# Optimization experiments

Hardware: AMD Instinct MI355X
Metric: run time of the kernel (lower is better)

## Reference

```python
import jax, jax.numpy as jnp
import numpy as np

N_NODES = 100000
N_EDGES = 1600000
N_GRAPHS = 64
IN_DIM = 256
OUT_DIM = 512
H1 = OUT_DIM // 4   # 128
H2 = OUT_DIM // 2   # 256


def glorot(key, shape):
    lim = float(np.sqrt(6.0 / (shape[0] + shape[1])))
    return jax.random.uniform(key, shape, jnp.float32, -lim, lim)


def setup_inputs() -> dict:
    key = jax.random.key(0)
    ks = jax.random.split(key, 8)
    x = jax.random.normal(ks[0], (N_NODES, IN_DIM), jnp.float32)
    edge_index = jax.random.randint(ks[1], (2, N_EDGES), 0, N_NODES, jnp.int64)
    batch = jnp.sort(jax.random.randint(ks[2], (N_NODES,), 0, N_GRAPHS, jnp.int64))
    return {
        'x': x,
        'edge_index': edge_index,
        'batch': batch,
        'W1': glorot(ks[3], (IN_DIM, H1)),
        'b1': jnp.zeros((H1,), jnp.float32),
        'W2': glorot(ks[4], (H1, H2)),
        'b2': jnp.zeros((H2,), jnp.float32),
        'fc_W': glorot(ks[5], (H2, OUT_DIM)),
        'fc_b': jnp.zeros((OUT_DIM,), jnp.float32),
    }


def gcn_conv(x, W, b, src, dst, n_nodes):
    # PyG GCNConv (default): add self-loops, sym-normalized aggregation of XW + bias
    h = x @ W                                   # [N, F_out] transform first (cheaper gather)
    ones = jnp.ones((src.shape[0],), h.dtype)
    deg = jax.ops.segment_sum(ones, dst, num_segments=n_nodes)  # includes self-loops
    dinv = jax.lax.rsqrt(jnp.maximum(deg, 1.0))
    norm = dinv[src] * dinv[dst]                # [E]
    msg = h[src] * norm[:, None]                # gather + scale
    out = jax.ops.segment_sum(msg, dst, num_segments=n_nodes)   # scatter-add
    return out + b


def reference(x, edge_index, batch, W1, b1, W2, b2, fc_W, fc_b):
    n = x.shape[0]
    loops = jnp.arange(n, dtype=edge_index.dtype)
    src = jnp.concatenate([edge_index[0], loops])
    dst = jnp.concatenate([edge_index[1], loops])

    h = jax.nn.relu(gcn_conv(x, W1, b1, src, dst, n))   # dropout = identity (eval)
    h = jax.nn.relu(gcn_conv(h, W2, b2, src, dst, n))

    # global_mean_pool over batch ids
    sums = jax.ops.segment_sum(h, batch, num_segments=N_GRAPHS)
    cnts = jax.ops.segment_sum(jnp.ones((n,), h.dtype), batch, num_segments=N_GRAPHS)
    pooled = sums / jnp.maximum(cnts, 1.0)[:, None]     # [B, H2]

    return jax.nn.relu(pooled @ fc_W + fc_b)            # [B, OUT_DIM]
```

## Files before the change

### kernel.cpp

```cpp
#include <hip/hip_runtime.h>
#include <hip/hip_bf16.h>
#include <cstdint>

#define N_NODES 100000
#define N_EDGES 1600000
#define N_GRAPHS 64
#define IN_DIM 256
#define HD1 128
#define HD2 256
#define OUT_DIM 512

#define NBUCK 196
#define NBLK  196
#define EPB   8192

typedef __bf16 bf16x8 __attribute__((ext_vector_type(8)));
typedef float f32x4 __attribute__((ext_vector_type(4)));

static __device__ __forceinline__ float bflo(uint32_t v) { return __uint_as_float(v << 16); }
static __device__ __forceinline__ float bfhi(uint32_t v) { return __uint_as_float(v & 0xffff0000u); }
static __device__ __forceinline__ uint32_t f2bf_bits(float f) {
    uint32_t u = __float_as_uint(f);
    return (u + 0x7fffu + ((u >> 16) & 1u)) >> 16;
}
static __device__ __forceinline__ uint32_t packbf(float a, float b) {
    return f2bf_bits(a) | (f2bf_bits(b) << 16);
}
static __device__ __forceinline__ float bf2f(uint16_t b) { return __uint_as_float(((uint32_t)b) << 16); }

__global__ void k_probe(const uint32_t* __restrict__ xw, const int* __restrict__ ei,
                        int* __restrict__ flags) {
    if (threadIdx.x != 0 || blockIdx.x != 0) return;
    int mid = 0;
    for (int i = 0; i < 64; i++) {
        uint32_t f = (xw[i] >> 23) & 0xFF;
        if (f >= 64 && f < 200) mid++;
    }
    flags[0] = (mid < 32) ? 1 : 0;
    int nz = 0;
    for (int i = 0; i < 64; i++) if (ei[2 * i + 1] != 0) nz++;
    flags[1] = (nz == 0) ? 1 : 0;
}

static __device__ __forceinline__ int ld_idx(const int* p, int i, int sh) { return p[i << sh]; }
static __device__ __forceinline__ float ld_f(const void* p, int i, int isbf) {
    return isbf ? bf2f(((const uint16_t*)p)[i]) : ((const float*)p)[i];
}

__global__ __launch_bounds__(256) void k_prep(const void* __restrict__ W1, const void* __restrict__ W2,
                                              const void* __restrict__ fcW, const void* __restrict__ b1,
                                              const void* __restrict__ b2, const void* __restrict__ fcb,
                                              uint16_t* __restrict__ W1F, uint16_t* __restrict__ W2F,
                                              uint16_t* __restrict__ fcWc, uint16_t* __restrict__ bc1,
                                              uint16_t* __restrict__ bc2, uint16_t* __restrict__ fcbc,
                                              const int* __restrict__ flags) {
    int i = blockIdx.x * 256 + threadIdx.x;
    int isbf = flags[0];
    if (i < 32768) {
        int j = i & 7, l = (i >> 3) & 63, nt = (i >> 9) & 1, ks = (i >> 10) & 7, n0g = (i >> 13) & 3;
        int k = ks * 32 + (l >> 4) * 8 + j;
        int n = n0g * 32 + nt * 16 + (l & 15);
        W1F[i] = (uint16_t)f2bf_bits(ld_f(W1, k * HD1 + n, isbf));
    } else if (i < 65536) {
        int j2 = i - 32768;
        int j = j2 & 7, l = (j2 >> 3) & 63, nt = (j2 >> 9) & 1, ks = (j2 >> 10) & 3, n0g = (j2 >> 12) & 7;
        int k = ks * 32 + (l >> 4) * 8 + j;
        int n = n0g * 32 + nt * 16 + (l & 15);
        W2F[j2] = (uint16_t)f2bf_bits(ld_f(W2, k * HD2 + n, isbf));
    } else if (i < 196608) {
        int j = i - 65536;
        fcWc[j] = (uint16_t)f2bf_bits(ld_f(fcW, j, isbf));
    } else if (i < 196736) {
        bc1[i - 196608] = (uint16_t)f2bf_bits(ld_f(b1, i - 196608, isbf));
    } else if (i < 196992) {
        bc2[i - 196736] = (uint16_t)f2bf_bits(ld_f(b2, i - 196736, isbf));
    } else if (i < 197504) {
        fcbc[i - 196992] = (uint16_t)f2bf_bits(ld_f(fcb, i - 196992, isbf));
    }
}


__global__ __launch_bounds__(256) void k_hist(const int* __restrict__ ei, int* __restrict__ bh,
                                              const int* __restrict__ flags) {
    __shared__ int h[NBUCK];
    int t = threadIdx.x, blk = blockIdx.x;
    if (t < NBUCK) h[t] = 0;
    __syncthreads();
    int sh = flags[1];
    int base = blk * EPB;
#pragma unroll
    for (int k = 0; k < EPB / 256; k++) {
        int e = base + k * 256 + t;
        if (e < N_EDGES) atomicAdd(&h[ld_idx(ei, N_EDGES + e, sh) >> 9], 1);
    }
    __syncthreads();
    if (t < NBUCK) bh[blk * NBUCK + t] = h[t];
}

__global__ __launch_bounds__(256) void k_colscan(const int* __restrict__ bh, int* __restrict__ bhoff,
                                                 int* __restrict__ bucket_cnt) {
    __shared__ int s[256];
    int b = blockIdx.x, t = threadIdx.x;
    int v = (t < NBLK) ? bh[t * NBUCK + b] : 0;
    s[t] = v; __syncthreads();
    for (int off = 1; off < 256; off <<= 1) {
        int x = (t >= off) ? s[t - off] : 0;
        __syncthreads();
        s[t] += x;
        __syncthreads();
    }
    if (t < NBLK) bhoff[t * NBUCK + b] = s[t] - v;
    if (t == 255) bucket_cnt[b] = s[255];
}

__global__ __launch_bounds__(256) void k_bscan(const int* __restrict__ bucket_cnt,
                                               int* __restrict__ bucket_base,
                                               int* __restrict__ row_ptr) {
    __shared__ int s[256];
    int t = threadIdx.x;
    int v = (t < NBUCK) ? bucket_cnt[t] : 0;
    s[t] = v; __syncthreads();
    for (int off = 1; off < 256; off <<= 1) {
        int x = (t >= off) ? s[t - off] : 0;
        __syncthreads();
        s[t] += x;
        __syncthreads();
    }
    if (t < NBUCK) bucket_base[t] = s[t] - v;
    if (t == NBUCK - 1) { bucket_base[NBUCK] = s[t]; row_ptr[N_NODES] = s[t]; }
}

__global__ __launch_bounds__(256) void k_part(const int* __restrict__ ei,
                                              const int* __restrict__ bucket_base,
                                              const int* __restrict__ bhoff,
                                              int* __restrict__ tmp,
                                              const int* __restrict__ flags) {
    __shared__ int cur[NBUCK];
    int t = threadIdx.x, blk = blockIdx.x;
    if (t < NBUCK) cur[t] = bucket_base[t] + bhoff[blk * NBUCK + t];
    __syncthreads();
    int sh = flags[1];
    int base = blk * EPB;
#pragma unroll
    for (int k = 0; k < EPB / 256; k++) {
        int e = base + k * 256 + t;
        if (e < N_EDGES) {
            int s = ld_idx(ei, e, sh), d = ld_idx(ei, N_EDGES + e, sh);
            int pos = atomicAdd(&cur[d >> 9], 1);
            tmp[pos] = (s << 9) | (d & 511);
        }
    }
}

__global__ __launch_bounds__(256) void k_bsort(const int* __restrict__ tmp,
                                               const int* __restrict__ bucket_base,
                                               int* __restrict__ csr_src,
                                               int* __restrict__ row_ptr,
                                               float* __restrict__ dinv) {
    __shared__ int h[512], a[512], c[512];
    int b = blockIdx.x, t = threadIdx.x;
    int beg = bucket_base[b], end = bucket_base[b + 1];
    h[t] = 0; h[t + 256] = 0;
    __syncthreads();
    for (int i = beg + t; i < end; i += 256) atomicAdd(&h[tmp[i] & 511], 1);
    __syncthreads();
    a[t] = h[t]; a[t + 256] = h[t + 256];
    __syncthreads();
    for (int off = 1; off < 512; off <<= 1) {
        int x0 = (t >= off) ? a[t - off] : 0;
        int x1 = ((t + 256) >= off) ? a[t + 256 - off] : 0;
        __syncthreads();
        a[t] += x0; a[t + 256] += x1;
        __syncthreads();
    }
#pragma unroll
    for (int u = 0; u < 2; u++) {
        int i = t + u * 256;
        int node = (b << 9) + i;
        int ex = a[i] - h[i];
        if (node < N_NODES) {
            row_ptr[node] = beg + ex;
            dinv[node] = rsqrtf((float)(h[i] + 1));
        }
        c[i] = ex;
    }
    __syncthreads();
    for (int i = beg + t; i < end; i += 256) {
        int e = tmp[i];
        int pos = atomicAdd(&c[e & 511], 1);
        csr_src[beg + pos] = e >> 9;
    }
}

#define GCNT_CHUNK 8
__global__ __launch_bounds__(256) void k_gcnt(const int* __restrict__ bat, int* __restrict__ gcnt,
                                              const int* __restrict__ flags) {
    __shared__ int h[N_GRAPHS];
    int t = threadIdx.x;
    if (t < N_GRAPHS) h[t] = 0;
    __syncthreads();
    int sh = flags[1];
    int base = (blockIdx.x * 256 + t) * GCNT_CHUNK;
    int cur = -1, run = 0;
#pragma unroll
    for (int u = 0; u < GCNT_CHUNK; u++) {
        int i = base + u;
        if (i < N_NODES) {
            int g = ld_idx(bat, i, sh);
            if (g == cur) run++;
            else { if (run) atomicAdd(&h[cur], run); cur = g; run = 1; }
        }
    }
    if (run) atomicAdd(&h[cur], run);
    __syncthreads();
    if (t < N_GRAPHS) { int v = h[t]; if (v) atomicAdd(&gcnt[t], v); }
}


__global__ __launch_bounds__(256) void k_gemm1(const void* __restrict__ Ain,
                                               const uint16_t* __restrict__ BF,
                                               uint16_t* __restrict__ C,
                                               const int* __restrict__ flags) {
    const int M = N_NODES, K = IN_DIM, N = HD1;
    int isbf = flags[0];
    int t = threadIdx.x;
    int wave = t >> 6, lane = t & 63;
    int quad = lane >> 4, l16 = lane & 15;
    int m0 = blockIdx.y * 128 + wave * 32;
    int n0 = blockIdx.x * 32;

    bf16x8 Bf[8][2];
#pragma unroll
    for (int ks = 0; ks < 8; ks++)
#pragma unroll
        for (int nt = 0; nt < 2; nt++)
            Bf[ks][nt] = *(const bf16x8*)(BF + ((((blockIdx.x * 8 + ks) * 2 + nt) << 6) + lane) * 8);

    int arow[2];
#pragma unroll
    for (int mt = 0; mt < 2; mt++) {
        int r = m0 + mt * 16 + l16;
        arow[mt] = r < M ? r : M - 1;
    }

    bf16x8 Af[8][2];
    if (isbf) {
        const uint16_t* Ab = (const uint16_t*)Ain;
#pragma unroll
        for (int ks = 0; ks < 8; ks++)
#pragma unroll
            for (int mt = 0; mt < 2; mt++)
                Af[ks][mt] = *(const bf16x8*)(Ab + arow[mt] * K + ks * 32 + quad * 8);
    } else {
        const float* Afp = (const float*)Ain;
#pragma unroll
        for (int ks = 0; ks < 8; ks++)
#pragma unroll
            for (int mt = 0; mt < 2; mt++) {
                const float* p = Afp + arow[mt] * K + ks * 32 + quad * 8;
                f32x4 f0 = *(const f32x4*)p, f1 = *(const f32x4*)(p + 4);
                union { uint16_t u[8]; bf16x8 v; } r;
#pragma unroll
                for (int j = 0; j < 4; j++) {
                    r.u[j]     = (uint16_t)f2bf_bits(f0[j]);
                    r.u[4 + j] = (uint16_t)f2bf_bits(f1[j]);
                }
                Af[ks][mt] = r.v;
            }
    }

    f32x4 acc[2][2];
#pragma unroll
    for (int a = 0; a < 2; a++)
#pragma unroll
        for (int b = 0; b < 2; b++) acc[a][b] = f32x4{0.f, 0.f, 0.f, 0.f};

#pragma unroll
    for (int ks = 0; ks < 8; ks++)
#pragma unroll
        for (int mt = 0; mt < 2; mt++)
#pragma unroll
            for (int nt = 0; nt < 2; nt++)
                acc[mt][nt] = __builtin_amdgcn_mfma_f32_16x16x32_bf16(Af[ks][mt], Bf[ks][nt], acc[mt][nt], 0, 0, 0);

#pragma unroll
    for (int mt = 0; mt < 2; mt++)
#pragma unroll
        for (int reg = 0; reg < 4; reg++) {
            int row = m0 + mt * 16 + quad * 4 + reg;
            if (row < M)
#pragma unroll
                for (int nt = 0; nt < 2; nt++)
                    C[row * N + n0 + nt * 16 + l16] = (uint16_t)f2bf_bits(acc[mt][nt][reg]);
        }
}


template <int WITH_BIAS_RELU>
__global__ __launch_bounds__(256) void k_agg(const uint16_t* __restrict__ Yin, uint16_t* __restrict__ Yout,
                                             const int* __restrict__ row_ptr, const int* __restrict__ csr_src,
                                             const float* __restrict__ dinv, const uint16_t* __restrict__ bias) {
    int node = blockIdx.x * 4 + (threadIdx.x >> 6);
    int l = threadIdx.x & 63;
    const uint32_t* Y32 = (const uint32_t*)Yin;

    float wd = dinv[node];
    uint32_t v = Y32[(size_t)node * 64 + l];
    float a0 = wd * bflo(v), a1 = wd * bfhi(v);

    int e0 = row_ptr[node], e1 = row_ptr[node + 1];
    for (int cb = e0; cb < e1; cb += 64) {
        int cnt = e1 - cb; if (cnt > 64) cnt = 64;
        int my_src = 0; uint32_t my_w = 0;
        if (l < cnt) { my_src = csr_src[cb + l]; my_w = __float_as_uint(dinv[my_src]); }
        int rounds = (cnt + 15) >> 4;
        for (int r = 0; r < rounds; r++) {
            int jb = r * 16;
            uint32_t vv[16];
#pragma unroll
            for (int t = 0; t < 16; t++) {
                int s = __builtin_amdgcn_readlane(my_src, jb + t);
                vv[t] = Y32[(size_t)s * 64 + l];
            }
#pragma unroll
            for (int t = 0; t < 16; t++) {
                float w = __uint_as_float(__builtin_amdgcn_readlane(my_w, jb + t));
                a0 += w * bflo(vv[t]);
                a1 += w * bfhi(vv[t]);
            }
        }
    }
    a0 *= wd; a1 *= wd;
    if (WITH_BIAS_RELU) {
        a0 = fmaxf(a0 + bf2f(bias[2 * l]), 0.f);
        a1 = fmaxf(a1 + bf2f(bias[2 * l + 1]), 0.f);
    }
    ((uint32_t*)Yout)[(size_t)node * 64 + l] = packbf(a0, a1);
}


__global__ __launch_bounds__(256) void k_gemm2_pool(const uint16_t* __restrict__ A,
                                                    const uint16_t* __restrict__ BF,
                                                    const uint16_t* __restrict__ bias,
                                                    const int* __restrict__ bat,
                                                    const int* __restrict__ flags,
                                                    float* __restrict__ pooled) {
    const int M = N_NODES, K = HD1;
    int t = threadIdx.x;
    int wave = t >> 6, lane = t & 63;
    int quad = lane >> 4, l16 = lane & 15;
    int m0 = blockIdx.y * 128 + wave * 32;
    int n0 = blockIdx.x * 32;

    bf16x8 Bf[4][2];
#pragma unroll
    for (int ks = 0; ks < 4; ks++)
#pragma unroll
        for (int nt = 0; nt < 2; nt++)
            Bf[ks][nt] = *(const bf16x8*)(BF + ((((blockIdx.x * 4 + ks) * 2 + nt) << 6) + lane) * 8);

    int arow[2];
#pragma unroll
    for (int mt = 0; mt < 2; mt++) {
        int r = m0 + mt * 16 + l16;
        arow[mt] = r < M ? r : M - 1;
    }

    bf16x8 Af[4][2];
#pragma unroll
    for (int ks = 0; ks < 4; ks++)
#pragma unroll
        for (int mt = 0; mt < 2; mt++)
            Af[ks][mt] = *(const bf16x8*)(A + arow[mt] * K + ks * 32 + quad * 8);

    f32x4 acc[2][2];
#pragma unroll
    for (int a = 0; a < 2; a++)
#pragma unroll
        for (int b = 0; b < 2; b++) acc[a][b] = f32x4{0.f, 0.f, 0.f, 0.f};

#pragma unroll
    for (int ks = 0; ks < 4; ks++)
#pragma unroll
        for (int mt = 0; mt < 2; mt++)
#pragma unroll
            for (int nt = 0; nt < 2; nt++)
                acc[mt][nt] = __builtin_amdgcn_mfma_f32_16x16x32_bf16(Af[ks][mt], Bf[ks][nt], acc[mt][nt], 0, 0, 0);

    int sh = flags[1];
    float bv[2];
#pragma unroll
    for (int nt = 0; nt < 2; nt++) bv[nt] = bf2f(bias[n0 + nt * 16 + l16]);

    if (m0 < M) {
        int gfirst = ld_idx(bat, m0, sh);
        int glast  = ld_idx(bat, m0 + 31, sh);
        if (gfirst == glast) {
#pragma unroll
            for (int nt = 0; nt < 2; nt++) {
                float s = 0.f;
#pragma unroll
                for (int mt = 0; mt < 2; mt++)
#pragma unroll
                    for (int reg = 0; reg < 4; reg++)
                        s += fmaxf(acc[mt][nt][reg] + bv[nt], 0.f);
                s += __shfl_xor(s, 16);
                s += __shfl_xor(s, 32);
                if (quad == 0)
                    atomicAdd(&pooled[gfirst * HD2 + n0 + nt * 16 + l16], s);
            }
        } else {
#pragma unroll
            for (int mt = 0; mt < 2; mt++) {
                int rb = m0 + mt * 16 + quad * 4;
#pragma unroll
                for (int reg = 0; reg < 4; reg++) {
                    int g = ld_idx(bat, rb + reg, sh);
#pragma unroll
                    for (int nt = 0; nt < 2; nt++)
                        atomicAdd(&pooled[g * HD2 + n0 + nt * 16 + l16],
                                  fmaxf(acc[mt][nt][reg] + bv[nt], 0.f));
                }
            }
        }
    }
}


__global__ __launch_bounds__(512) void k_final(const float* __restrict__ pooled, const int* __restrict__ gcnt,
                                               const uint16_t* __restrict__ fcWc, const uint16_t* __restrict__ fcbc,
                                               void* __restrict__ out, const int* __restrict__ flags) {
    __shared__ float pm[HD2];
    int g = blockIdx.x, t = threadIdx.x;
    if (t < HD2) pm[t] = pooled[g * HD2 + t] / fmaxf((float)gcnt[g], 1.0f);
    __syncthreads();
    float acc = bf2f(fcbc[t]);
    for (int k = 0; k < HD2; k++) acc = fmaf(pm[k], bf2f(fcWc[k * OUT_DIM + t]), acc);
    acc = fmaxf(acc, 0.f);
    if (flags[0]) ((uint16_t*)out)[g * OUT_DIM + t] = (uint16_t)f2bf_bits(acc);
    else          ((float*)out)[g * OUT_DIM + t] = acc;
}


extern "C" void kernel_launch(void* const* d_in, const int* in_sizes, int n_in,
                              void* d_out, int out_size, void* d_ws, size_t ws_size,
                              hipStream_t stream) {
    const void* x   = d_in[0];
    const int*  ei  = (const int*)d_in[1];
    const int*  bat = (const int*)d_in[2];
    const void* W1  = d_in[3];
    const void* b1  = d_in[4];
    const void* W2  = d_in[5];
    const void* b2  = d_in[6];
    const void* fcW = d_in[7];
    const void* fcb = d_in[8];

    char* ws = (char*)d_ws;
    size_t off = 0;
    auto alloc = [&](size_t bytes) -> void* {
        void* p = ws + off;
        off += (bytes + 255) & ~(size_t)255;
        return p;
    };
    uint16_t* buf0 = (uint16_t*)alloc((size_t)N_NODES * HD1 * 2);
    uint16_t* Hb   = (uint16_t*)alloc((size_t)N_NODES * HD1 * 2);
    int*   row_ptr = (int*)alloc((N_NODES + 1) * 4);
    int*   csr_src = (int*)alloc((size_t)N_EDGES * 4);
    int*   tmp     = (int*)alloc((size_t)N_EDGES * 4);
    int*   bh      = (int*)alloc(NBLK * NBUCK * 4);
    int*   bhoff   = (int*)alloc(NBLK * NBUCK * 4);
    int*   bucket_cnt  = (int*)alloc(NBUCK * 4);
    int*   bucket_base = (int*)alloc((NBUCK + 1) * 4);
    float* dinv    = (float*)alloc(N_NODES * 4);
    int*   gcnt    = (int*)alloc(N_GRAPHS * 4);
    float* pooled  = (float*)alloc(N_GRAPHS * HD2 * 4);
    uint16_t* W1T  = (uint16_t*)alloc(IN_DIM * HD1 * 2);
    uint16_t* W2T  = (uint16_t*)alloc(HD1 * HD2 * 2);
    uint16_t* bc1  = (uint16_t*)alloc(HD1 * 2);
    uint16_t* bc2  = (uint16_t*)alloc(HD2 * 2);
    uint16_t* fcWc = (uint16_t*)alloc(HD2 * OUT_DIM * 2);
    uint16_t* fcbc = (uint16_t*)alloc(OUT_DIM * 2);
    int*   flags   = (int*)alloc(64 * 4);

    uint16_t* Y1 = buf0;
    uint16_t* Zb = buf0;

    hipMemsetAsync(gcnt, 0, N_GRAPHS * 4, stream);
    hipMemsetAsync(pooled, 0, N_GRAPHS * HD2 * 4, stream);

    k_probe<<<1, 64, 0, stream>>>((const uint32_t*)x, ei, flags);

    k_prep<<<(197504 + 255) / 256, 256, 0, stream>>>(W1, W2, fcW, b1, b2, fcb,
                                                     W1T, W2T, fcWc, bc1, bc2, fcbc, flags);

    k_hist<<<NBLK, 256, 0, stream>>>(ei, bh, flags);
    k_colscan<<<NBUCK, 256, 0, stream>>>(bh, bhoff, bucket_cnt);
    k_bscan<<<1, 256, 0, stream>>>(bucket_cnt, bucket_base, row_ptr);
    k_part<<<NBLK, 256, 0, stream>>>(ei, bucket_base, bhoff, tmp, flags);
    k_bsort<<<NBUCK, 256, 0, stream>>>(tmp, bucket_base, csr_src, row_ptr, dinv);

    k_gcnt<<<(N_NODES + 256 * GCNT_CHUNK - 1) / (256 * GCNT_CHUNK), 256, 0, stream>>>(bat, gcnt, flags);

    k_gemm1<<<dim3(4, (N_NODES + 127) / 128), 256, 0, stream>>>(x, W1T, Y1, flags);
    k_agg<1><<<N_NODES / 4, 256, 0, stream>>>(Y1, Hb, row_ptr, csr_src, dinv, bc1);

    k_agg<0><<<N_NODES / 4, 256, 0, stream>>>(Hb, Zb, row_ptr, csr_src, dinv, nullptr);
    k_gemm2_pool<<<dim3(8, (N_NODES + 127) / 128), 256, 0, stream>>>(Zb, W2T, bc2, bat, flags, pooled);

    k_final<<<N_GRAPHS, 512, 0, stream>>>(pooled, gcnt, fcWc, fcbc, d_out, flags);
}
```

Measured before the change: 450.9 us.

## Stage GEMM A tiles in swizzled LDS and share them across output-column waves

```diff
diff --git a/kernel.cpp b/kernel.cpp
--- a/kernel.cpp
+++ b/kernel.cpp
@@ -27,6 +27,11 @@
     return f2bf_bits(a) | (f2bf_bits(b) << 16);
 }
 static __device__ __forceinline__ float bf2f(uint16_t b) { return __uint_as_float(((uint32_t)b) << 16); }
+
+static __device__ __forceinline__ void gl_lds16(const void* g, void* l) {
+    __builtin_amdgcn_global_load_lds((const __attribute__((address_space(1))) uint32_t*)g,
+                                     (__attribute__((address_space(3))) uint32_t*)l, 16, 0, 0);
+}
 
 __global__ void k_probe(const uint32_t* __restrict__ xw, const int* __restrict__ ei,
                         int* __restrict__ flags) {
@@ -221,70 +226,75 @@
                                                const uint16_t* __restrict__ BF,
                                                uint16_t* __restrict__ C,
                                                const int* __restrict__ flags) {
-    const int M = N_NODES, K = IN_DIM, N = HD1;
+    __shared__ __align__(16) uint16_t As[64 * 256];
+    const int M = N_NODES, N = HD1;
     int isbf = flags[0];
     int t = threadIdx.x;
     int wave = t >> 6, lane = t & 63;
     int quad = lane >> 4, l16 = lane & 15;
-    int m0 = blockIdx.y * 128 + wave * 32;
-    int n0 = blockIdx.x * 32;
+    int m0 = blockIdx.x * 64;
+    int n0 = wave * 32;
 
     bf16x8 Bf[8][2];
 #pragma unroll
     for (int ks = 0; ks < 8; ks++)
 #pragma unroll
         for (int nt = 0; nt < 2; nt++)
-            Bf[ks][nt] = *(const bf16x8*)(BF + ((((blockIdx.x * 8 + ks) * 2 + nt) << 6) + lane) * 8);
-
-    int arow[2];
-#pragma unroll
-    for (int mt = 0; mt < 2; mt++) {
-        int r = m0 + mt * 16 + l16;
-        arow[mt] = r < M ? r : M - 1;
-    }
-
-    bf16x8 Af[8][2];
+            Bf[ks][nt] = *(const bf16x8*)(BF + ((((wave * 8 + ks) * 2 + nt) << 6) + lane) * 8);
+
     if (isbf) {
-        const uint16_t* Ab = (const uint16_t*)Ain;
-#pragma unroll
-        for (int ks = 0; ks < 8; ks++)
-#pragma unroll
-            for (int mt = 0; mt < 2; mt++)
-                Af[ks][mt] = *(const bf16x8*)(Ab + arow[mt] * K + ks * 32 + quad * 8);
+        const uint8_t* Xb = (const uint8_t*)Ain;
+#pragma unroll
+        for (int i = 0; i < 8; i++) {
+            int o = (i * 256 + t) * 16;
+            int r = o >> 9, c = o & 511;
+            int rg = m0 + r; if (rg >= M) rg = M - 1;
+            gl_lds16(Xb + (size_t)rg * 512 + (c ^ ((r & 7) << 4)), (uint8_t*)As + o);
+        }
     } else {
-        const float* Afp = (const float*)Ain;
-#pragma unroll
-        for (int ks = 0; ks < 8; ks++)
-#pragma unroll
-            for (int mt = 0; mt < 2; mt++) {
-                const float* p = Afp + arow[mt] * K + ks * 32 + quad * 8;
-                f32x4 f0 = *(const f32x4*)p, f1 = *(const f32x4*)(p + 4);
-                union { uint16_t u[8]; bf16x8 v; } r;
-#pragma unroll
-                for (int j = 0; j < 4; j++) {
-                    r.u[j]     = (uint16_t)f2bf_bits(f0[j]);
-                    r.u[4 + j] = (uint16_t)f2bf_bits(f1[j]);
-                }
-                Af[ks][mt] = r.v;
+        const float* Xf = (const float*)Ain;
+#pragma unroll
+        for (int i = 0; i < 8; i++) {
+            int o = (i * 256 + t) * 16;
+            int r = o >> 9, c = (o & 511) ^ ((r & 7) << 4);
+            int rg = m0 + r; if (rg >= M) rg = M - 1;
+            const float* p = Xf + (size_t)rg * 256 + (c >> 1);
+            f32x4 f0 = *(const f32x4*)p, f1 = *(const f32x4*)(p + 4);
+            union { uint16_t u[8]; bf16x8 v; } rr;
+#pragma unroll
+            for (int j = 0; j < 4; j++) {
+                rr.u[j]     = (uint16_t)f2bf_bits(f0[j]);
+                rr.u[4 + j] = (uint16_t)f2bf_bits(f1[j]);
             }
-    }
-
-    f32x4 acc[2][2];
-#pragma unroll
-    for (int a = 0; a < 2; a++)
+            *(bf16x8*)((uint8_t*)As + o) = rr.v;
+        }
+    }
+    __syncthreads();
+
+    f32x4 acc[4][2];
+#pragma unroll
+    for (int a = 0; a < 4; a++)
 #pragma unroll
         for (int b = 0; b < 2; b++) acc[a][b] = f32x4{0.f, 0.f, 0.f, 0.f};
 
 #pragma unroll
-    for (int ks = 0; ks < 8; ks++)
-#pragma unroll
-        for (int mt = 0; mt < 2; mt++)
+    for (int ks = 0; ks < 8; ks++) {
+        bf16x8 af[4];
+#pragma unroll
+        for (int mt = 0; mt < 4; mt++) {
+            int r = mt * 16 + l16;
+            int cb = (ks * 64 + quad * 16) ^ ((r & 7) << 4);
+            af[mt] = *(const bf16x8*)((const uint8_t*)As + r * 512 + cb);
+        }
+#pragma unroll
+        for (int mt = 0; mt < 4; mt++)
 #pragma unroll
             for (int nt = 0; nt < 2; nt++)
-                acc[mt][nt] = __builtin_amdgcn_mfma_f32_16x16x32_bf16(Af[ks][mt], Bf[ks][nt], acc[mt][nt], 0, 0, 0);
-
-#pragma unroll
-    for (int mt = 0; mt < 2; mt++)
+                acc[mt][nt] = __builtin_amdgcn_mfma_f32_16x16x32_bf16(af[mt], Bf[ks][nt], acc[mt][nt], 0, 0, 0);
+    }
+
+#pragma unroll
+    for (int mt = 0; mt < 4; mt++)
 #pragma unroll
         for (int reg = 0; reg < 4; reg++) {
             int row = m0 + mt * 16 + quad * 4 + reg;
@@ -339,83 +349,88 @@
 }
 
 
-__global__ __launch_bounds__(256) void k_gemm2_pool(const uint16_t* __restrict__ A,
+__global__ __launch_bounds__(512) void k_gemm2_pool(const uint16_t* __restrict__ A,
                                                     const uint16_t* __restrict__ BF,
                                                     const uint16_t* __restrict__ bias,
                                                     const int* __restrict__ bat,
                                                     const int* __restrict__ flags,
                                                     float* __restrict__ pooled) {
-    const int M = N_NODES, K = HD1;
+    __shared__ __align__(16) uint16_t As[64 * 128];
+    const int M = N_NODES;
     int t = threadIdx.x;
     int wave = t >> 6, lane = t & 63;
     int quad = lane >> 4, l16 = lane & 15;
-    int m0 = blockIdx.y * 128 + wave * 32;
-    int n0 = blockIdx.x * 32;
+    int m0 = blockIdx.x * 64;
+    int n0 = wave * 32;
 
     bf16x8 Bf[4][2];
 #pragma unroll
     for (int ks = 0; ks < 4; ks++)
 #pragma unroll
         for (int nt = 0; nt < 2; nt++)
-            Bf[ks][nt] = *(const bf16x8*)(BF + ((((blockIdx.x * 4 + ks) * 2 + nt) << 6) + lane) * 8);
-
-    int arow[2];
-#pragma unroll
-    for (int mt = 0; mt < 2; mt++) {
-        int r = m0 + mt * 16 + l16;
-        arow[mt] = r < M ? r : M - 1;
-    }
-
-    bf16x8 Af[4][2];
-#pragma unroll
-    for (int ks = 0; ks < 4; ks++)
-#pragma unroll
-        for (int mt = 0; mt < 2; mt++)
-            Af[ks][mt] = *(const bf16x8*)(A + arow[mt] * K + ks * 32 + quad * 8);
-
-    f32x4 acc[2][2];
-#pragma unroll
-    for (int a = 0; a < 2; a++)
+            Bf[ks][nt] = *(const bf16x8*)(BF + ((((wave * 4 + ks) * 2 + nt) << 6) + lane) * 8);
+
+#pragma unroll
+    for (int i = 0; i < 2; i++) {
+        int o = (i * 512 + t) * 16;
+        int r = o >> 8, c = o & 255;
+        int rg = m0 + r; if (rg >= M) rg = M - 1;
+        gl_lds16((const uint8_t*)A + (size_t)rg * 256 + (c ^ ((r & 7) << 4)), (uint8_t*)As + o);
+    }
+    __syncthreads();
+
+    f32x4 acc[4][2];
+#pragma unroll
+    for (int a = 0; a < 4; a++)
 #pragma unroll
         for (int b = 0; b < 2; b++) acc[a][b] = f32x4{0.f, 0.f, 0.f, 0.f};
 
 #pragma unroll
-    for (int ks = 0; ks < 4; ks++)
-#pragma unroll
-        for (int mt = 0; mt < 2; mt++)
+    for (int ks = 0; ks < 4; ks++) {
+        bf16x8 af[4];
+#pragma unroll
+        for (int mt = 0; mt < 4; mt++) {
+            int r = mt * 16 + l16;
+            int cb = (ks * 64 + quad * 16) ^ ((r & 7) << 4);
+            af[mt] = *(const bf16x8*)((const uint8_t*)As + r * 256 + cb);
+        }
+#pragma unroll
+        for (int mt = 0; mt < 4; mt++)
 #pragma unroll
             for (int nt = 0; nt < 2; nt++)
-                acc[mt][nt] = __builtin_amdgcn_mfma_f32_16x16x32_bf16(Af[ks][mt], Bf[ks][nt], acc[mt][nt], 0, 0, 0);
+                acc[mt][nt] = __builtin_amdgcn_mfma_f32_16x16x32_bf16(af[mt], Bf[ks][nt], acc[mt][nt], 0, 0, 0);
+    }
 
     int sh = flags[1];
     float bv[2];
 #pragma unroll
     for (int nt = 0; nt < 2; nt++) bv[nt] = bf2f(bias[n0 + nt * 16 + l16]);
 
-    if (m0 < M) {
-        int gfirst = ld_idx(bat, m0, sh);
-        int glast  = ld_idx(bat, m0 + 31, sh);
-        if (gfirst == glast) {
-#pragma unroll
-            for (int nt = 0; nt < 2; nt++) {
-                float s = 0.f;
-#pragma unroll
-                for (int mt = 0; mt < 2; mt++)
-#pragma unroll
-                    for (int reg = 0; reg < 4; reg++)
-                        s += fmaxf(acc[mt][nt][reg] + bv[nt], 0.f);
-                s += __shfl_xor(s, 16);
-                s += __shfl_xor(s, 32);
-                if (quad == 0)
-                    atomicAdd(&pooled[gfirst * HD2 + n0 + nt * 16 + l16], s);
-            }
-        } else {
-#pragma unroll
-            for (int mt = 0; mt < 2; mt++) {
-                int rb = m0 + mt * 16 + quad * 4;
-#pragma unroll
-                for (int reg = 0; reg < 4; reg++) {
-                    int g = ld_idx(bat, rb + reg, sh);
+    int last = m0 + 63 < M ? m0 + 63 : M - 1;
+    int gfirst = ld_idx(bat, m0, sh);
+    int glast  = ld_idx(bat, last, sh);
+    if ((m0 + 63 < M) && gfirst == glast) {
+#pragma unroll
+        for (int nt = 0; nt < 2; nt++) {
+            float s = 0.f;
+#pragma unroll
+            for (int mt = 0; mt < 4; mt++)
+#pragma unroll
+                for (int reg = 0; reg < 4; reg++)
+                    s += fmaxf(acc[mt][nt][reg] + bv[nt], 0.f);
+            s += __shfl_xor(s, 16);
+            s += __shfl_xor(s, 32);
+            if (quad == 0)
+                atomicAdd(&pooled[gfirst * HD2 + n0 + nt * 16 + l16], s);
+        }
+    } else {
+#pragma unroll
+        for (int mt = 0; mt < 4; mt++) {
+#pragma unroll
+            for (int reg = 0; reg < 4; reg++) {
+                int row = m0 + mt * 16 + quad * 4 + reg;
+                if (row < M) {
+                    int g = ld_idx(bat, row, sh);
 #pragma unroll
                     for (int nt = 0; nt < 2; nt++)
                         atomicAdd(&pooled[g * HD2 + n0 + nt * 16 + l16],
@@ -501,11 +516,11 @@
 
     k_gcnt<<<(N_NODES + 256 * GCNT_CHUNK - 1) / (256 * GCNT_CHUNK), 256, 0, stream>>>(bat, gcnt, flags);
 
-    k_gemm1<<<dim3(4, (N_NODES + 127) / 128), 256, 0, stream>>>(x, W1T, Y1, flags);
+    k_gemm1<<<(N_NODES + 63) / 64, 256, 0, stream>>>(x, W1T, Y1, flags);
     k_agg<1><<<N_NODES / 4, 256, 0, stream>>>(Y1, Hb, row_ptr, csr_src, dinv, bc1);
 
     k_agg<0><<<N_NODES / 4, 256, 0, stream>>>(Hb, Zb, row_ptr, csr_src, dinv, nullptr);
-    k_gemm2_pool<<<dim3(8, (N_NODES + 127) / 128), 256, 0, stream>>>(Zb, W2T, bc2, bat, flags, pooled);
+    k_gemm2_pool<<<(N_NODES + 63) / 64, 512, 0, stream>>>(Zb, W2T, bc2, bat, flags, pooled);
 
     k_final<<<N_GRAPHS, 512, 0, stream>>>(pooled, gcnt, fcWc, fcbc, d_out, flags);
 }
```

After: 417.8 us. 7.3% less time.
